# Performance work log

Hardware: AMD Instinct MI355X
Metric: run time of the kernel (lower is better)

Reference implementation:

```python
import jax, jax.numpy as jnp
import numpy as np

S, HID, H, KV, D = 2048, 3584, 16, 8, 256
WINDOW = 1024
SOFTCAP = 50.0
SCALING = 256 ** (-0.5)  # query_pre_attn_scalar ** -0.5
EPS = 1e-6
ROPE_THETA = 10000.0


def _rope_tables(seq_len, dim, theta):
    inv_freq = 1.0 / (theta ** (np.arange(0, dim, 2, dtype=np.float32) / dim))
    t = np.arange(seq_len, dtype=np.float32)
    freqs = np.outer(t, inv_freq)            # [S, D/2]
    emb = np.concatenate([freqs, freqs], -1)  # [S, D]
    return jnp.asarray(np.cos(emb)), jnp.asarray(np.sin(emb))


def setup_inputs() -> dict:
    key = jax.random.key(0)
    ks = jax.random.split(key, 3)
    hidden_states = jax.random.normal(ks[0], (S, HID), jnp.float32)
    w_qkv = jax.random.normal(ks[1], (HID, (H + 2 * KV) * D), jnp.float32) * (HID ** -0.5)
    w_o = jax.random.normal(ks[2], (H * D, HID), jnp.float32) * ((H * D) ** -0.5)
    q_norm_w = jnp.zeros((D,), jnp.float32)  # gemma norm stores weight as (1 + w)
    k_norm_w = jnp.zeros((D,), jnp.float32)
    cos, sin = _rope_tables(S, D, ROPE_THETA)
    return {"hidden_states": hidden_states, "w_qkv": w_qkv, "w_o": w_o,
            "q_norm_w": q_norm_w, "k_norm_w": k_norm_w, "cos": cos, "sin": sin}


def _rms_norm(x, w):
    # gemma-style: fp32 norm, scale by (1 + w); x: [S, h, D]
    xf = x.astype(jnp.float32)
    var = jnp.mean(xf * xf, axis=-1, keepdims=True)
    return (xf * jax.lax.rsqrt(var + EPS) * (1.0 + w)).astype(x.dtype)


def _rotate_half(x):
    x1, x2 = jnp.split(x, 2, axis=-1)
    return jnp.concatenate([-x2, x1], axis=-1)


def _apply_rope(x, cos, sin):
    # x: [S, h, D]; cos/sin: [S, D]
    c = cos[:, None, :]
    s = sin[:, None, :]
    return x * c + _rotate_half(x) * s


def reference(hidden_states, w_qkv, w_o, q_norm_w, k_norm_w, cos, sin):
    qkv = hidden_states @ w_qkv                      # [S, (H+2KV)*D]
    q = qkv[:, : H * D].reshape(S, H, D)
    k = qkv[:, H * D: (H + KV) * D].reshape(S, KV, D)
    v = qkv[:, (H + KV) * D:].reshape(S, KV, D)

    q = _rms_norm(q, q_norm_w)                       # gemma3 q_norm
    k = _rms_norm(k, k_norm_w)                       # gemma3 k_norm
    q = _apply_rope(q, cos, sin)
    k = _apply_rope(k, cos, sin)

    # GQA: expand KV heads to H
    rep = H // KV
    k = jnp.repeat(k, rep, axis=1)                   # [S, H, D]
    v = jnp.repeat(v, rep, axis=1)

    scores = jnp.einsum('shd,thd->hst', q, k) * SCALING  # [H, S, S]
    scores = SOFTCAP * jnp.tanh(scores / SOFTCAP)        # logit softcapping

    i = jnp.arange(S)[:, None]
    j = jnp.arange(S)[None, :]
    allowed = (j <= i) & ((i - j) < WINDOW)              # causal + sliding window
    scores = jnp.where(allowed[None], scores, jnp.float32(-1e30))

    attn = jax.nn.softmax(scores, axis=-1)
    out = jnp.einsum('hst,thd->shd', attn, v).reshape(S, H * D)
    return out @ w_o                                     # [S, HID]
```

## Files before the change

kernel.cpp:

```cpp
#include <hip/hip_runtime.h>
#include <hip/hip_bf16.h>
#include <math.h>

typedef __attribute__((ext_vector_type(8))) short short8;
typedef __attribute__((ext_vector_type(4))) float floatx4;
typedef unsigned short u16;

typedef __attribute__((address_space(1))) const void* gas_ptr;
typedef __attribute__((address_space(3))) void* las_ptr;

__device__ __forceinline__ float bf2f(u16 h) {
  union { unsigned u; float f; } v; v.u = ((unsigned)h) << 16; return v.f;
}
__device__ __forceinline__ u16 f2bf(float f) {
  union { float f; unsigned u; } v; v.f = f;
  unsigned r = v.u + 0x7FFFu + ((v.u >> 16) & 1u);
  return (u16)(r >> 16);
}
__device__ __forceinline__ float ldf_dyn(const void* p, size_t i, bool f32) {
  return f32 ? ((const float*)p)[i] : bf2f(((const u16*)p)[i]);
}
__device__ __forceinline__ short8 load8_dyn(const void* p, size_t idx, bool f32) {
  if (f32) {
    const float* f = (const float*)p;
    float4 a = *(const float4*)(f + idx);
    float4 b = *(const float4*)(f + idx + 4);
    short8 r;
    r[0] = (short)f2bf(a.x); r[1] = (short)f2bf(a.y);
    r[2] = (short)f2bf(a.z); r[3] = (short)f2bf(a.w);
    r[4] = (short)f2bf(b.x); r[5] = (short)f2bf(b.y);
    r[6] = (short)f2bf(b.z); r[7] = (short)f2bf(b.w);
    return r;
  }
  return *(const short8*)((const u16*)p + idx);
}
__device__ __forceinline__ void gl_lds16(const u16* g, u16* l) {
  __builtin_amdgcn_global_load_lds((gas_ptr)g, (las_ptr)l, 16, 0, 0);
}

__global__ void probe_dtype_kernel(const void* hidden, int* flag) {
  __shared__ int cnt;
  if (threadIdx.x == 0) cnt = 0;
  __syncthreads();
  const u16* h = (const u16*)hidden;
  int local = 0;
  for (int i = threadIdx.x; i < 8192; i += 256) {
    u16 u = h[i];
    int e = (u >> 7) & 0xFF;
    if ((e >= 64 && e <= 160) || (u & 0x7FFF) == 0) local++;
  }
  atomicAdd(&cnt, local);
  __syncthreads();
  if (threadIdx.x == 0) *flag = (cnt < 7700) ? 1 : 0;
}

__global__ __launch_bounds__(256) void convert_dyn_kernel(
    const void* __restrict__ src, u16* __restrict__ dst, size_t n,
    const int* __restrict__ flagp)
{
  const bool f32 = (*flagp != 0);
  size_t i = ((size_t)blockIdx.x * 256 + threadIdx.x) * 8;
  if (i < n) *(short8*)(dst + i) = load8_dyn(src, i, f32);
}

__global__ __launch_bounds__(256) void transpose_dyn_kernel(
    const void* __restrict__ src, u16* __restrict__ dst, int R, int C,
    const int* __restrict__ flagp)
{
  const bool f32 = (*flagp != 0);
  const int c0 = blockIdx.x * 64, r0 = blockIdx.y * 64;
  __shared__ __attribute__((aligned(16))) u16 T[64][72];
  const int tid = threadIdx.x;
#pragma unroll
  for (int i = 0; i < 2; i++) {
    int t = tid + i * 256;
    int r = t >> 3, cc = (t & 7) << 3;
    *(short8*)(&T[r][cc]) = load8_dyn(src, (size_t)(r0 + r) * C + c0 + cc, f32);
  }
  __syncthreads();
#pragma unroll
  for (int i = 0; i < 2; i++) {
    int t = tid + i * 256;
    int cr = t >> 3, rc = (t & 7) << 3;
    __attribute__((aligned(16))) u16 tmp[8];
#pragma unroll
    for (int j = 0; j < 8; j++) tmp[j] = T[rc + j][cr];
    *(short8*)(dst + (size_t)(c0 + cr) * R + r0 + rc) = *(const short8*)tmp;
  }
}

__device__ __forceinline__ int aoff(int wm, int lane15, int quad, int mi, int ks) {
  int c = (ks * 64 + quad * 16) ^ ((lane15 & 12) << 2) ^ ((mi & 1) << 6);
  return wm * 8192 + (mi * 16 + lane15) * 64 + (c >> 1);
}
__device__ __forceinline__ int boff(int wn, int lane15, int quad, int ni, int ks) {
  int c = (ks * 64 + quad * 16) ^ ((lane15 & 12) << 2) ^ ((ni & 1) << 6);
  return 16384 + (wn >> 1) * 8192 + ((wn & 1) * 64 + ni * 16 + lane15) * 64 + (c >> 1);
}

#define BAR() __builtin_amdgcn_s_barrier()
#define SCB() __builtin_amdgcn_sched_barrier(0)
#define LGKM0() do { asm volatile("s_waitcnt lgkmcnt(0)" ::: "memory"); SCB(); } while (0)
#define VMW(n) do { asm volatile("s_waitcnt vmcnt(" #n ")" ::: "memory"); SCB(); } while (0)

#define STG_A(s, h, t) do { \
  gl_lds16(pa + (size_t)((h) * 128) * K + (size_t)(t) * 64, \
           lA + (s) * 32768 + (h) * 8192); \
  gl_lds16(pa + (size_t)((h) * 128 + 64) * K + (size_t)(t) * 64, \
           lA + (s) * 32768 + (h) * 8192 + 4096); \
} while (0)
#define STG_B(s, h, t) do { \
  gl_lds16(pb + (size_t)((h) * 128) * K + (size_t)(t) * 64, \
           lB + (s) * 32768 + (h) * 8192); \
  gl_lds16(pb + (size_t)((h) * 128 + 64) * K + (size_t)(t) * 64, \
           lB + (s) * 32768 + (h) * 8192 + 4096); \
} while (0)

#define RD_FA(s, miH) do { \
  _Pragma("unroll") \
  for (int m2 = 0; m2 < 4; m2++) { \
    fa[m2][0] = *(const short8*)(LDS + (s) * 32768 + aoff(wm, lane15, quad, (miH) * 4 + m2, 0)); \
    fa[m2][1] = *(const short8*)(LDS + (s) * 32768 + aoff(wm, lane15, quad, (miH) * 4 + m2, 1)); \
  } \
} while (0)
#define RD_FB(s, niH) do { \
  _Pragma("unroll") \
  for (int n2 = 0; n2 < 2; n2++) { \
    fb[n2][0] = *(const short8*)(LDS + (s) * 32768 + boff(wn, lane15, quad, (niH) * 2 + n2, 0)); \
    fb[n2][1] = *(const short8*)(LDS + (s) * 32768 + boff(wn, lane15, quad, (niH) * 2 + n2, 1)); \
  } \
} while (0)
#define MFMA_Q(miH, niH) do { \
  __builtin_amdgcn_s_setprio(1); \
  _Pragma("unroll") \
  for (int m2 = 0; m2 < 4; m2++) \
    _Pragma("unroll") \
    for (int n2 = 0; n2 < 2; n2++) { \
      acc[(miH) * 4 + m2][(niH) * 2 + n2] = __builtin_amdgcn_mfma_f32_16x16x32_bf16( \
          fa[m2][0], fb[n2][0], acc[(miH) * 4 + m2][(niH) * 2 + n2], 0, 0, 0); \
      acc[(miH) * 4 + m2][(niH) * 2 + n2] = __builtin_amdgcn_mfma_f32_16x16x32_bf16( \
          fa[m2][1], fb[n2][1], acc[(miH) * 4 + m2][(niH) * 2 + n2], 0, 0, 0); \
    } \
  __builtin_amdgcn_s_setprio(0); \
  SCB(); \
} while (0)

__global__ __launch_bounds__(512, 2) void gemm8p_kernel(
    const u16* __restrict__ A, const u16* __restrict__ BT, u16* __restrict__ C,
    int M, int N, int K)
{
  __shared__ __attribute__((aligned(16))) u16 LDS[65536];
  const int tid = threadIdx.x;
  const int wave = tid >> 6, lane = tid & 63;
  const int lane15 = lane & 15, quad = lane >> 4;
  const int wm = wave >> 2, wn = wave & 3;
  const int m0 = blockIdx.y * 256, n0 = blockIdx.x * 256;

  const int rloc = wave * 8 + (lane >> 3);
  const int s3 = ((lane >> 5) & 1) | ((wave & 1) << 1) | (((wave >> 1) & 1) << 2);
  const int csw = ((lane & 7) * 8) ^ (s3 << 3);
  const u16* pa = A + (size_t)(m0 + rloc) * K + csw;
  const u16* pb = BT + (size_t)(n0 + rloc) * K + csw;
  u16* lA = LDS + wave * 512;
  u16* lB = LDS + 16384 + wave * 512;

  floatx4 acc[8][4];
#pragma unroll
  for (int i = 0; i < 8; i++)
#pragma unroll
    for (int j = 0; j < 4; j++) acc[i][j] = (floatx4){0.f, 0.f, 0.f, 0.f};
  short8 fa[4][2], fb[2][2];

  const int NT = K >> 6, NI = NT >> 1;

  STG_A(0, 0, 0); STG_A(0, 1, 0); STG_B(0, 0, 0); STG_B(0, 1, 0); STG_A(1, 0, 1);
  VMW(2);
  BAR();

  for (int i = 0; i < NI - 1; i++) {
    const int t1 = 2 * i + 1, t2 = 2 * i + 2, t3 = 2 * i + 3;
    RD_FA(0, 0); RD_FB(0, 0); STG_A(1, 1, t1);
    BAR(); LGKM0(); MFMA_Q(0, 0); BAR();
    RD_FB(0, 1); STG_B(1, 0, t1);
    BAR(); LGKM0(); MFMA_Q(0, 1); BAR();
    RD_FA(0, 1); STG_B(1, 1, t1);
    BAR(); LGKM0(); MFMA_Q(1, 1); BAR();
    RD_FB(0, 0); STG_A(0, 0, t2);
    BAR(); LGKM0(); MFMA_Q(1, 0); VMW(2); BAR();
    RD_FA(1, 0); RD_FB(1, 0); STG_A(0, 1, t2);
    BAR(); LGKM0(); MFMA_Q(0, 0); BAR();
    RD_FB(1, 1); STG_B(0, 0, t2);
    BAR(); LGKM0(); MFMA_Q(0, 1); BAR();
    RD_FA(1, 1); STG_B(0, 1, t2);
    BAR(); LGKM0(); MFMA_Q(1, 1); BAR();
    RD_FB(1, 0); STG_A(1, 0, t3);
    BAR(); LGKM0(); MFMA_Q(1, 0); VMW(2); BAR();
  }

  {
    const int tL = NT - 1;
    RD_FA(0, 0); RD_FB(0, 0); STG_A(1, 1, tL);
    BAR(); LGKM0(); MFMA_Q(0, 0); BAR();
    RD_FB(0, 1); STG_B(1, 0, tL);
    BAR(); LGKM0(); MFMA_Q(0, 1); BAR();
    RD_FA(0, 1); STG_B(1, 1, tL);
    BAR(); LGKM0(); MFMA_Q(1, 1); BAR();
    RD_FB(0, 0);
    BAR(); LGKM0(); MFMA_Q(1, 0); VMW(0); BAR();
    RD_FA(1, 0); RD_FB(1, 0);
    BAR(); LGKM0(); MFMA_Q(0, 0); BAR();
    RD_FB(1, 1);
    BAR(); LGKM0(); MFMA_Q(0, 1); BAR();
    RD_FA(1, 1);
    BAR(); LGKM0(); MFMA_Q(1, 1); BAR();
    RD_FB(1, 0);
    BAR(); LGKM0(); MFMA_Q(1, 0);
  }

#pragma unroll
  for (int mi = 0; mi < 8; mi++)
#pragma unroll
    for (int rr = 0; rr < 4; rr++) {
      int m = m0 + wm * 128 + mi * 16 + quad * 4 + rr;
      u16* crow = C + (size_t)m * N + n0 + wn * 64;
#pragma unroll
      for (int ni = 0; ni < 4; ni++) crow[ni * 16 + lane15] = f2bf(acc[mi][ni][rr]);
    }
}

__global__ __launch_bounds__(256) void gemm_bt_kernel(
    const u16* __restrict__ A, const u16* __restrict__ BT, void* __restrict__ C,
    int M, int N, int K, const int* __restrict__ flagp, int cdyn)
{
  __shared__ __attribute__((aligned(16))) u16 As[128 * 32];
  __shared__ __attribute__((aligned(16))) u16 Bs[128 * 32];
  const int tid = threadIdx.x;
  const int wave = tid >> 6, lane = tid & 63;
  const int lane15 = lane & 15, quad = lane >> 4;
  const int wr = (wave >> 1) * 64, wc = (wave & 1) * 64;
  const int m0 = blockIdx.y * 128, n0 = blockIdx.x * 128;

  const int ch0 = wave * 64 + lane;
  const int ch1 = ch0 + 256;
  const int sr0 = ch0 >> 2, sk0 = (ch0 & 3) << 3;
  const int sr1 = ch1 >> 2, sk1 = (ch1 & 3) << 3;
  u16* ldsA0 = &As[wave * 512];
  u16* ldsA1 = &As[2048 + wave * 512];
  u16* ldsB0 = &Bs[wave * 512];
  u16* ldsB1 = &Bs[2048 + wave * 512];
  const u16* pa0 = A + (size_t)(m0 + sr0) * K + sk0;
  const u16* pa1 = A + (size_t)(m0 + sr1) * K + sk1;
  const u16* pb0 = BT + (size_t)(n0 + sr0) * K + sk0;
  const u16* pb1 = BT + (size_t)(n0 + sr1) * K + sk1;

  floatx4 zero = {0.0f, 0.0f, 0.0f, 0.0f};
  floatx4 acc[4][4];
#pragma unroll
  for (int i = 0; i < 4; i++)
#pragma unroll
    for (int j = 0; j < 4; j++) acc[i][j] = zero;

  for (int k0 = 0; k0 < K; k0 += 32) {
    gl_lds16(pa0, ldsA0); gl_lds16(pa1, ldsA1);
    gl_lds16(pb0, ldsB0); gl_lds16(pb1, ldsB1);
    pa0 += 32; pa1 += 32; pb0 += 32; pb1 += 32;
    __syncthreads();
    short8 af[4], bfr[4];
#pragma unroll
    for (int mi = 0; mi < 4; mi++)
      af[mi] = *(const short8*)(&As[(wr + mi * 16 + lane15) * 32 + quad * 8]);
#pragma unroll
    for (int ni = 0; ni < 4; ni++)
      bfr[ni] = *(const short8*)(&Bs[(wc + ni * 16 + lane15) * 32 + quad * 8]);
#pragma unroll
    for (int mi = 0; mi < 4; mi++)
#pragma unroll
      for (int ni = 0; ni < 4; ni++)
        acc[mi][ni] = __builtin_amdgcn_mfma_f32_16x16x32_bf16(
            af[mi], bfr[ni], acc[mi][ni], 0, 0, 0);
    __syncthreads();
  }
  const bool cf32 = cdyn && (*flagp != 0);
  if (cf32) {
    float* Cf = (float*)C;
#pragma unroll
    for (int mi = 0; mi < 4; mi++)
#pragma unroll
      for (int r = 0; r < 4; r++) {
        int m = m0 + wr + mi * 16 + quad * 4 + r;
        float* crow = Cf + (size_t)m * N + n0 + wc;
#pragma unroll
        for (int ni = 0; ni < 4; ni++) crow[ni * 16 + lane15] = acc[mi][ni][r];
      }
  } else {
    u16* Cb = (u16*)C;
#pragma unroll
    for (int mi = 0; mi < 4; mi++)
#pragma unroll
      for (int r = 0; r < 4; r++) {
        int m = m0 + wr + mi * 16 + quad * 4 + r;
        u16* crow = Cb + (size_t)m * N + n0 + wc;
#pragma unroll
        for (int ni = 0; ni < 4; ni++) crow[ni * 16 + lane15] = f2bf(acc[mi][ni][r]);
      }
  }
}

__global__ __launch_bounds__(256) void normrope_kernel(
    u16* __restrict__ qkv, const void* __restrict__ qw,
    const void* __restrict__ kw, const void* __restrict__ cosb,
    const void* __restrict__ sinb, const int* __restrict__ flagp)
{
  const bool f32 = (*flagp != 0);
  const int s = blockIdx.x;
  const int wave = threadIdx.x >> 6, lane = threadIdx.x & 63;
  const int hh = blockIdx.y * 4 + wave;
  const int col = (hh < 16) ? hh * 256 : 4096 + (hh - 16) * 256;
  const void* w = (hh < 16) ? qw : kw;
  u16* row = qkv + (size_t)s * 8192 + col;

  float x[4];
#pragma unroll
  for (int j = 0; j < 4; j++) x[j] = bf2f(row[lane + j * 64]);

  float ss = x[0] * x[0] + x[1] * x[1] + x[2] * x[2] + x[3] * x[3];
#pragma unroll
  for (int off = 32; off > 0; off >>= 1) ss += __shfl_xor(ss, off);
  float inv = rsqrtf(ss * (1.0f / 256.0f) + 1e-6f);

  float y[4];
#pragma unroll
  for (int j = 0; j < 4; j++)
    y[j] = x[j] * inv * (1.0f + ldf_dyn(w, lane + j * 64, f32));
  float rot[4] = {-y[2], -y[3], y[0], y[1]};
#pragma unroll
  for (int j = 0; j < 4; j++) {
    int d = lane + j * 64;
    float c = ldf_dyn(cosb, (size_t)s * 256 + d, f32);
    float sn = ldf_dyn(sinb, (size_t)s * 256 + d, f32);
    row[d] = f2bf(y[j] * c + rot[j] * sn);
  }
}

__global__ __launch_bounds__(256) void vtrans_kernel(
    const u16* __restrict__ qkv, u16* __restrict__ vT)
{
  const int s0 = blockIdx.x * 64, d0 = blockIdx.y * 64, kv = blockIdx.z;
  __shared__ __attribute__((aligned(16))) u16 T[64][72];
  const int tid = threadIdx.x;
#pragma unroll
  for (int i = 0; i < 2; i++) {
    int c = tid + i * 256;
    int r = c >> 3, dc = (c & 7) << 3;
    *(short8*)(&T[r][dc]) =
        *(const short8*)(qkv + (size_t)(s0 + r) * 8192 + 6144 + kv * 256 + d0 + dc);
  }
  __syncthreads();
#pragma unroll
  for (int i = 0; i < 2; i++) {
    int c = tid + i * 256;
    int dr = c >> 3, sc = (c & 7) << 3;
    __attribute__((aligned(16))) u16 tmp[8];
#pragma unroll
    for (int j = 0; j < 8; j++) tmp[j] = T[sc + j][dr];
    *(short8*)(vT + (size_t)kv * 524288 + (size_t)(d0 + dr) * 2048 + s0 + sc) =
        *(const short8*)tmp;
  }
}

__global__ __launch_bounds__(256) void attn_kernel(
    const u16* __restrict__ qkv, const u16* __restrict__ vT,
    u16* __restrict__ aout)
{
  const int h = blockIdx.y, kvh = h >> 1;
  const int q0 = blockIdx.x * 64;
  const int tid = threadIdx.x;
  const int wave = tid >> 6, lane = tid & 63;
  const int lane15 = lane & 15, quad = lane >> 4;

  __shared__ __attribute__((aligned(16))) u16 KVs[256 * 72];
  __shared__ __attribute__((aligned(16))) u16 Ps[4][16 * 72];

  short8 aq[8];
  const u16* qrow = qkv + (size_t)(q0 + wave * 16 + lane15) * 8192 + h * 256;
#pragma unroll
  for (int kt = 0; kt < 8; kt++)
    aq[kt] = *(const short8*)(qrow + kt * 32 + quad * 8);

  floatx4 zero = {0.0f, 0.0f, 0.0f, 0.0f};
  floatx4 accO[16];
#pragma unroll
  for (int i = 0; i < 16; i++) accO[i] = zero;
  float lR[4] = {0.0f, 0.0f, 0.0f, 0.0f};

  const int iRow = q0 + wave * 16 + quad * 4;
  const int kb_lo = (q0 >= 1023) ? ((q0 - 1023) >> 6) : 0;
  const int kb_hi = q0 >> 6;

  for (int kb = kb_lo; kb <= kb_hi; kb++) {
    const int t0 = kb << 6;
#pragma unroll
    for (int i = 0; i < 8; i++) {
      int c = tid + i * 256;
      int r = c >> 5, dc = (c & 31) << 3;
      *(short8*)(&KVs[r * 264 + dc]) =
          *(const short8*)(qkv + (size_t)(t0 + r) * 8192 + 4096 + kvh * 256 + dc);
    }
    __syncthreads();

    const int relHi = q0 + 16 * wave + 15 - t0;
    const int relLo = q0 + 16 * wave - 1023 - t0;
    const int niHiR = relHi >> 4;
    const int niHi = (niHiR > 3) ? 3 : niHiR;
    int niLo = relLo >> 4; if (niLo < 0) niLo = 0;
    const int ktHiR = relHi >> 5;
    const int ktHi = (ktHiR > 1) ? 1 : ktHiR;
    int ktLo = relLo >> 5; if (ktLo < 0) ktLo = 0;

    float pv[4][4];
#pragma unroll
    for (int ni = 0; ni < 4; ni++) {
      if (ni < niLo || ni > niHi) {
        pv[ni][0] = pv[ni][1] = pv[ni][2] = pv[ni][3] = 0.0f;
        continue;
      }
      floatx4 sAcc = zero;
#pragma unroll
      for (int kt = 0; kt < 8; kt++) {
        short8 bk = *(const short8*)(&KVs[(ni * 16 + lane15) * 264 + kt * 32 + quad * 8]);
        sAcc = __builtin_amdgcn_mfma_f32_16x16x32_bf16(aq[kt], bk, sAcc, 0, 0, 0);
      }
#pragma unroll
      for (int r = 0; r < 4; r++) {
        float x = sAcc[r] * 0.00125f;
        float ax = __builtin_fabsf(x);
        float e2 = __expf(ax + ax);
        float t = 1.0f - 2.0f * __builtin_amdgcn_rcpf(e2 + 1.0f);
        float sv = copysignf(t, x) * 50.0f;
        int i_ = iRow + r;
        int j_ = t0 + ni * 16 + lane15;
        bool ok = (j_ <= i_) && (i_ - j_ < 1024);
        pv[ni][r] = ok ? __expf(sv) : 0.0f;
      }
    }
#pragma unroll
    for (int r = 0; r < 4; r++)
      lR[r] += pv[0][r] + pv[1][r] + pv[2][r] + pv[3][r];

#pragma unroll
    for (int ni = 0; ni < 4; ni++)
#pragma unroll
      for (int r = 0; r < 4; r++)
        Ps[wave][(quad * 4 + r) * 72 + ni * 16 + lane15] = f2bf(pv[ni][r]);
    __syncthreads();

#pragma unroll
    for (int i = 0; i < 8; i++) {
      int c = tid + i * 256;
      int dr = c >> 3, tc = (c & 7) << 3;
      *(short8*)(&KVs[dr * 72 + tc]) =
          *(const short8*)(vT + (size_t)kvh * 524288 + (size_t)dr * 2048 + t0 + tc);
    }
    __syncthreads();

#pragma unroll
    for (int ktile = 0; ktile < 2; ktile++) {
      if (ktile < ktLo || ktile > ktHi) continue;
      short8 ap = *(const short8*)(&Ps[wave][lane15 * 72 + ktile * 32 + quad * 8]);
#pragma unroll
      for (int ni = 0; ni < 16; ni++) {
        short8 bv = *(const short8*)(&KVs[(ni * 16 + lane15) * 72 + ktile * 32 + quad * 8]);
        accO[ni] = __builtin_amdgcn_mfma_f32_16x16x32_bf16(ap, bv, accO[ni], 0, 0, 0);
      }
    }
    __syncthreads();
  }

#pragma unroll
  for (int r = 0; r < 4; r++) {
    float l = lR[r];
    l += __shfl_xor(l, 1);
    l += __shfl_xor(l, 2);
    l += __shfl_xor(l, 4);
    l += __shfl_xor(l, 8);
    float invl = 1.0f / l;
    u16* orow = aout + (size_t)(q0 + wave * 16 + quad * 4 + r) * 4096 + h * 256;
#pragma unroll
    for (int ni = 0; ni < 16; ni++)
      orow[ni * 16 + lane15] = f2bf(accO[ni][r] * invl);
  }
}

extern "C" void kernel_launch(void* const* d_in, const int* in_sizes, int n_in,
                              void* d_out, int out_size, void* d_ws, size_t ws_size,
                              hipStream_t stream)
{
  const void* hidden = d_in[0];
  const void* w_qkv  = d_in[1];
  const void* w_o    = d_in[2];
  const void* q_w    = d_in[3];
  const void* k_w    = d_in[4];
  const void* cosb   = d_in[5];
  const void* sinb   = d_in[6];

  char* ws = (char*)d_ws;
  int* flag = (int*)ws;                                   ws += 256;
  u16* qkv  = (u16*)ws;  ws += (size_t)2048 * 8192 * 2;
  u16* vT   = (u16*)ws;  ws += (size_t)8 * 256 * 2048 * 2;
  u16* aout = (u16*)ws;  ws += (size_t)2048 * 4096 * 2;
  u16* hb   = (u16*)ws;  ws += (size_t)2048 * 3584 * 2;
  u16* wT   = (u16*)ws;

  probe_dtype_kernel<<<1, 256, 0, stream>>>(hidden, flag);
  convert_dyn_kernel<<<3584, 256, 0, stream>>>(hidden, hb, (size_t)2048 * 3584, flag);
  transpose_dyn_kernel<<<dim3(128, 56), 256, 0, stream>>>(w_qkv, wT, 3584, 8192, flag);
  gemm8p_kernel<<<dim3(32, 8), 512, 0, stream>>>(hb, wT, qkv, 2048, 8192, 3584);
  normrope_kernel<<<dim3(2048, 6), 256, 0, stream>>>(qkv, q_w, k_w, cosb, sinb, flag);
  transpose_dyn_kernel<<<dim3(56, 64), 256, 0, stream>>>(w_o, wT, 4096, 3584, flag);
  vtrans_kernel<<<dim3(32, 4, 8), 256, 0, stream>>>(qkv, vT);
  attn_kernel<<<dim3(32, 16), 256, 0, stream>>>(qkv, vT, aout);
  gemm_bt_kernel<<<dim3(28, 16), 256, 0, stream>>>(aout, wT, d_out, 2048, 3584, 4096, flag, 1);
}
```

Measured before the change: 626.7 us.

## Restructure 8-phase GEMM staging with finer-grained loads and cached B fragments

Splits global-to-LDS staging into 64-row units issued earlier and more evenly across the eight phases, and changes the LDS swizzle to a simpler XOR on column chunks. B fragments are now kept for both halves, so the fourth MFMA quarter reuses registers instead of re-reading LDS. The aim is deeper prefetch overlap and fewer LDS reads. The cost is more VGPRs for fragments and more intricate vmcnt accounting, which risks correctness or lower occupancy.

```diff
diff --git a/kernel.cpp b/kernel.cpp
--- a/kernel.cpp
+++ b/kernel.cpp
@@ -89,45 +89,32 @@
   }
 }
 
-__device__ __forceinline__ int aoff(int wm, int lane15, int quad, int mi, int ks) {
-  int c = (ks * 64 + quad * 16) ^ ((lane15 & 12) << 2) ^ ((mi & 1) << 6);
-  return wm * 8192 + (mi * 16 + lane15) * 64 + (c >> 1);
-}
-__device__ __forceinline__ int boff(int wn, int lane15, int quad, int ni, int ks) {
-  int c = (ks * 64 + quad * 16) ^ ((lane15 & 12) << 2) ^ ((ni & 1) << 6);
-  return 16384 + (wn >> 1) * 8192 + ((wn & 1) * 64 + ni * 16 + lane15) * 64 + (c >> 1);
-}
-
 #define BAR() __builtin_amdgcn_s_barrier()
 #define SCB() __builtin_amdgcn_sched_barrier(0)
 #define LGKM0() do { asm volatile("s_waitcnt lgkmcnt(0)" ::: "memory"); SCB(); } while (0)
 #define VMW(n) do { asm volatile("s_waitcnt vmcnt(" #n ")" ::: "memory"); SCB(); } while (0)
 
-#define STG_A(s, h, t) do { \
-  gl_lds16(pa + (size_t)((h) * 128) * K + (size_t)(t) * 64, \
-           lA + (s) * 32768 + (h) * 8192); \
-  gl_lds16(pa + (size_t)((h) * 128 + 64) * K + (size_t)(t) * 64, \
-           lA + (s) * 32768 + (h) * 8192 + 4096); \
-} while (0)
-#define STG_B(s, h, t) do { \
-  gl_lds16(pb + (size_t)((h) * 128) * K + (size_t)(t) * 64, \
-           lB + (s) * 32768 + (h) * 8192); \
-  gl_lds16(pb + (size_t)((h) * 128 + 64) * K + (size_t)(t) * 64, \
-           lB + (s) * 32768 + (h) * 8192 + 4096); \
-} while (0)
+#define STG_AU(s, u, t) \
+  gl_lds16(pa + (size_t)((u) * 64) * K + (size_t)(t) * 64, \
+           ldsw + (s) * 32768 + (u) * 4096)
+#define STG_BU(s, u, t) \
+  gl_lds16(pb + (size_t)((u) * 64) * K + (size_t)(t) * 64, \
+           ldsw + (s) * 32768 + 16384 + (u) * 4096)
 
 #define RD_FA(s, miH) do { \
   _Pragma("unroll") \
   for (int m2 = 0; m2 < 4; m2++) { \
-    fa[m2][0] = *(const short8*)(LDS + (s) * 32768 + aoff(wm, lane15, quad, (miH) * 4 + m2, 0)); \
-    fa[m2][1] = *(const short8*)(LDS + (s) * 32768 + aoff(wm, lane15, quad, (miH) * 4 + m2, 1)); \
+    const u16* _r = LDS + (s) * 32768 + wm * 8192 + (miH) * 4096 + m2 * 1024 + lane15 * 64; \
+    fa[m2][0] = *(const short8*)(_r + colA0); \
+    fa[m2][1] = *(const short8*)(_r + colA1); \
   } \
 } while (0)
 #define RD_FB(s, niH) do { \
   _Pragma("unroll") \
   for (int n2 = 0; n2 < 2; n2++) { \
-    fb[n2][0] = *(const short8*)(LDS + (s) * 32768 + boff(wn, lane15, quad, (niH) * 2 + n2, 0)); \
-    fb[n2][1] = *(const short8*)(LDS + (s) * 32768 + boff(wn, lane15, quad, (niH) * 2 + n2, 1)); \
+    const u16* _r = LDS + (s) * 32768 + 16384 + wn * 4096 + (niH) * 2048 + n2 * 1024 + lane15 * 64; \
+    fb[niH][n2][0] = *(const short8*)(_r + colA0); \
+    fb[niH][n2][1] = *(const short8*)(_r + colA1); \
   } \
 } while (0)
 #define MFMA_Q(miH, niH) do { \
@@ -137,9 +124,9 @@
     _Pragma("unroll") \
     for (int n2 = 0; n2 < 2; n2++) { \
       acc[(miH) * 4 + m2][(niH) * 2 + n2] = __builtin_amdgcn_mfma_f32_16x16x32_bf16( \
-          fa[m2][0], fb[n2][0], acc[(miH) * 4 + m2][(niH) * 2 + n2], 0, 0, 0); \
+          fa[m2][0], fb[niH][n2][0], acc[(miH) * 4 + m2][(niH) * 2 + n2], 0, 0, 0); \
       acc[(miH) * 4 + m2][(niH) * 2 + n2] = __builtin_amdgcn_mfma_f32_16x16x32_bf16( \
-          fa[m2][1], fb[n2][1], acc[(miH) * 4 + m2][(niH) * 2 + n2], 0, 0, 0); \
+          fa[m2][1], fb[niH][n2][1], acc[(miH) * 4 + m2][(niH) * 2 + n2], 0, 0, 0); \
     } \
   __builtin_amdgcn_s_setprio(0); \
   SCB(); \
@@ -157,64 +144,78 @@
   const int m0 = blockIdx.y * 256, n0 = blockIdx.x * 256;
 
   const int rloc = wave * 8 + (lane >> 3);
-  const int s3 = ((lane >> 5) & 1) | ((wave & 1) << 1) | (((wave >> 1) & 1) << 2);
-  const int csw = ((lane & 7) * 8) ^ (s3 << 3);
+  const int sxor = (((lane >> 3) & 1) << 2) | ((wave & 1) << 1) | ((lane >> 5) & 1);
+  const int csw = ((lane & 7) ^ sxor) * 8;
   const u16* pa = A + (size_t)(m0 + rloc) * K + csw;
   const u16* pb = BT + (size_t)(n0 + rloc) * K + csw;
-  u16* lA = LDS + wave * 512;
-  u16* lB = LDS + 16384 + wave * 512;
+  u16* ldsw = LDS + wave * 512;
+
+  const int swz = ((lane15 & 1) << 2) | ((lane15 >> 2) & 3);
+  const int colA0 = (quad ^ swz) * 8;
+  const int colA1 = ((4 + quad) ^ swz) * 8;
 
   floatx4 acc[8][4];
 #pragma unroll
   for (int i = 0; i < 8; i++)
 #pragma unroll
     for (int j = 0; j < 4; j++) acc[i][j] = (floatx4){0.f, 0.f, 0.f, 0.f};
-  short8 fa[4][2], fb[2][2];
+  short8 fa[4][2], fb[2][2][2];
 
   const int NT = K >> 6, NI = NT >> 1;
 
-  STG_A(0, 0, 0); STG_A(0, 1, 0); STG_B(0, 0, 0); STG_B(0, 1, 0); STG_A(1, 0, 1);
-  VMW(2);
+  STG_AU(0, 0, 0); STG_AU(0, 2, 0);
+  STG_BU(0, 0, 0); STG_BU(0, 1, 0);
+  STG_BU(0, 2, 0); STG_BU(0, 3, 0);
+  STG_AU(0, 1, 0); STG_AU(0, 3, 0);
+  STG_AU(1, 0, 1); STG_AU(1, 2, 1);
+  STG_BU(1, 0, 1); STG_BU(1, 1, 1);
+  STG_BU(1, 2, 1); STG_BU(1, 3, 1);
+  VMW(8);
   BAR();
 
   for (int i = 0; i < NI - 1; i++) {
     const int t1 = 2 * i + 1, t2 = 2 * i + 2, t3 = 2 * i + 3;
-    RD_FA(0, 0); RD_FB(0, 0); STG_A(1, 1, t1);
+    RD_FA(0, 0); RD_FB(0, 0);
+    STG_AU(1, 1, t1); STG_AU(1, 3, t1);
     BAR(); LGKM0(); MFMA_Q(0, 0); BAR();
-    RD_FB(0, 1); STG_B(1, 0, t1);
-    BAR(); LGKM0(); MFMA_Q(0, 1); BAR();
-    RD_FA(0, 1); STG_B(1, 1, t1);
+    RD_FB(0, 1);
+    STG_AU(0, 0, t2); STG_AU(0, 2, t2);
+    BAR(); LGKM0(); MFMA_Q(0, 1); VMW(10); BAR();
+    RD_FA(0, 1);
+    STG_BU(0, 0, t2); STG_BU(0, 1, t2);
     BAR(); LGKM0(); MFMA_Q(1, 1); BAR();
-    RD_FB(0, 0); STG_A(0, 0, t2);
-    BAR(); LGKM0(); MFMA_Q(1, 0); VMW(2); BAR();
-    RD_FA(1, 0); RD_FB(1, 0); STG_A(0, 1, t2);
+    STG_BU(0, 2, t2); STG_BU(0, 3, t2);
+    BAR(); MFMA_Q(1, 0); VMW(8); BAR();
+    RD_FA(1, 0); RD_FB(1, 0);
+    STG_AU(0, 1, t2); STG_AU(0, 3, t2);
     BAR(); LGKM0(); MFMA_Q(0, 0); BAR();
-    RD_FB(1, 1); STG_B(0, 0, t2);
-    BAR(); LGKM0(); MFMA_Q(0, 1); BAR();
-    RD_FA(1, 1); STG_B(0, 1, t2);
+    RD_FB(1, 1);
+    STG_AU(1, 0, t3); STG_AU(1, 2, t3);
+    BAR(); LGKM0(); MFMA_Q(0, 1); VMW(10); BAR();
+    RD_FA(1, 1);
+    STG_BU(1, 0, t3); STG_BU(1, 1, t3);
     BAR(); LGKM0(); MFMA_Q(1, 1); BAR();
-    RD_FB(1, 0); STG_A(1, 0, t3);
-    BAR(); LGKM0(); MFMA_Q(1, 0); VMW(2); BAR();
+    STG_BU(1, 2, t3); STG_BU(1, 3, t3);
+    BAR(); MFMA_Q(1, 0); VMW(8); BAR();
   }
 
   {
     const int tL = NT - 1;
-    RD_FA(0, 0); RD_FB(0, 0); STG_A(1, 1, tL);
+    RD_FA(0, 0); RD_FB(0, 0);
+    STG_AU(1, 1, tL); STG_AU(1, 3, tL);
     BAR(); LGKM0(); MFMA_Q(0, 0); BAR();
-    RD_FB(0, 1); STG_B(1, 0, tL);
-    BAR(); LGKM0(); MFMA_Q(0, 1); BAR();
-    RD_FA(0, 1); STG_B(1, 1, tL);
+    RD_FB(0, 1);
+    BAR(); LGKM0(); MFMA_Q(0, 1); VMW(8); BAR();
+    RD_FA(0, 1);
     BAR(); LGKM0(); MFMA_Q(1, 1); BAR();
-    RD_FB(0, 0);
-    BAR(); LGKM0(); MFMA_Q(1, 0); VMW(0); BAR();
+    BAR(); MFMA_Q(1, 0); VMW(2); BAR();
     RD_FA(1, 0); RD_FB(1, 0);
     BAR(); LGKM0(); MFMA_Q(0, 0); BAR();
     RD_FB(1, 1);
-    BAR(); LGKM0(); MFMA_Q(0, 1); BAR();
+    BAR(); LGKM0(); MFMA_Q(0, 1); VMW(0); BAR();
     RD_FA(1, 1);
     BAR(); LGKM0(); MFMA_Q(1, 1); BAR();
-    RD_FB(1, 0);
-    BAR(); LGKM0(); MFMA_Q(1, 0);
+    BAR(); MFMA_Q(1, 0);
   }
 
 #pragma unroll
```

New measurement: 616.9 us. Within noise of the previous version (-1.6%).
